# Performance work log

Measured on AMD Instinct MI355X. Metric: run time of the kernel, lower is better.

The kernel has to match this reference:

```python
import jax, jax.numpy as jnp
import numpy as np

NFRAMES, BS, LATENT = 196, 128, 1024
E = 16            # number of object types (experts)
NJOINTS = 128     # max joints -> padded width
NFEATS = 6
INPUT_FEATS = NJOINTS * NFEATS  # 768


def setup_inputs() -> dict:
    key = jax.random.key(0)
    k1, k2, k3, k4 = jax.random.split(key, 4)
    output = jax.random.normal(k1, (NFRAMES, BS, LATENT), dtype=jnp.float32)
    object_types = jax.random.randint(k2, (BS,), 0, E)
    # stacked per-type Linear params, zero-padded to INPUT_FEATS
    W = jax.random.normal(k3, (E, LATENT, INPUT_FEATS), dtype=jnp.float32) * (1.0 / np.sqrt(LATENT))
    b = jax.random.normal(k4, (E, INPUT_FEATS), dtype=jnp.float32) * 0.01
    # valid joints per type in [8, NJOINTS]
    joint_counts = jax.random.randint(jax.random.fold_in(key, 7), (E,), 8, NJOINTS + 1)
    return {"output": output, "object_types": object_types, "W": W, "b": b,
            "joint_counts": joint_counts}


def reference(output, object_types, W, b, joint_counts):
    # per-expert valid output width and column mask [E, INPUT_FEATS]
    feat_counts = joint_counts * NFEATS
    col_mask = (jnp.arange(INPUT_FEATS)[None, :] < feat_counts[:, None]).astype(output.dtype)
    # gather per-sample expert params: Wg [BS, LATENT, F], bg/mg [BS, F]
    Wg = W[object_types]
    bg = b[object_types]
    mg = col_mask[object_types]
    # y[t,b,f] = sum_d output[t,b,d] * Wg[b,d,f] + bg[b,f], zero-padded past valid width
    y = (jnp.einsum('tbd,bdf->tbf', output, Wg) + bg[None]) * mg[None]
    y = y.reshape(NFRAMES, BS, NJOINTS, NFEATS)
    return jnp.transpose(y, (1, 2, 3, 0))  # (bs, njoints, nfeats, nframes)
```

## Files before the change

kernel.cpp:

```cpp
#include <hip/hip_runtime.h>
#include <hip/hip_bf16.h>


#define NFRAMES 196
#define TPAD    208
#define BSZ     128
#define DLAT    1024
#define FIN     768
#define BM      128
#define BK      32
#define KSTEPS  (DLAT / BK)
#define MTILES  (FIN / BM)
#define NFRAG   (TPAD / 16)
#define NTHREADS 256

typedef short bf16x8 __attribute__((ext_vector_type(8)));
typedef short s16x4  __attribute__((ext_vector_type(4)));
typedef float f32x4  __attribute__((ext_vector_type(4)));

__device__ __forceinline__ int swz(int r) { return ((r >> 2) & 3) ^ ((r >> 1) & 1); }

__device__ __forceinline__ short f2bf(float f) {
    __hip_bfloat16 h = __float2bfloat16(f);
    return __builtin_bit_cast(short, h);
}

#define BAR() do { asm volatile("s_waitcnt lgkmcnt(0)" ::: "memory"); \
                   __builtin_amdgcn_s_barrier(); } while (0)

__global__ __launch_bounds__(NTHREADS, 2)
void fused_expert_gemm(const float* __restrict__ X,
                       const int*   __restrict__ otypes,
                       const float* __restrict__ W,
                       const float* __restrict__ Bias,
                       const int*   __restrict__ jc,
                       float*       __restrict__ out)
{
    __shared__ short As[BM * BK];
    __shared__ short Bs[TPAD * BK];

    const int hw      = blockIdx.x;
    const int logical = (hw & 7) * ((MTILES * BSZ) / 8) + (hw >> 3);
    const int b       = logical / MTILES;
    const int mt      = logical - b * MTILES;
    const int m0      = mt * BM;

    const int tid = threadIdx.x;
    const int e   = otypes[b];

    const int kb = tid >> 5;
    const int mb = tid & 31;
    const int kq = tid & 7;
    const int rp = tid >> 3;

    const f32x4* __restrict__ Xv = reinterpret_cast<const f32x4*>(X);
    const f32x4* __restrict__ Wv = reinterpret_cast<const f32x4*>(W);
    const f32x4 fzero = {0.f, 0.f, 0.f, 0.f};

    f32x4 wa[4];
    f32x4 xb[7];

    const int wave = tid >> 6;
    const int lane = tid & 63;
    const int lr   = lane & 15;
    const int g    = lane >> 4;

    f32x4 acc[2][NFRAG];
    #pragma unroll
    for (int i = 0; i < 2; ++i)
        #pragma unroll
        for (int j = 0; j < NFRAG; ++j) acc[i][j] = fzero;

    auto load_stage = [&](int k0) {
        #pragma unroll
        for (int i = 0; i < 4; ++i)
            wa[i] = Wv[(size_t)(e * DLAT + k0 + kb * 4 + i) * (FIN / 4) + (m0 >> 2) + mb];
        #pragma unroll
        for (int p = 0; p < 7; ++p) {
            const int n = p * 32 + rp;
            if (n < NFRAMES)
                xb[p] = Xv[((size_t)n * BSZ + b) * (DLAT / 4) + (k0 >> 2) + kq];
            else
                xb[p] = fzero;
        }
    };

    auto write_stage = [&]() {
        #pragma unroll
        for (int j = 0; j < 4; ++j) {
            const int mm = (mb + j) & 3;
            const int m  = mb * 4 + mm;
            s16x4 v;
            v[0] = f2bf(wa[0][mm]); v[1] = f2bf(wa[1][mm]);
            v[2] = f2bf(wa[2][mm]); v[3] = f2bf(wa[3][mm]);
            const int ea = m * 32 + (((kb >> 1) ^ swz(m)) << 3) + (kb & 1) * 4;
            *reinterpret_cast<s16x4*>(&As[ea]) = v;
        }
        #pragma unroll
        for (int p = 0; p < 7; ++p) {
            const int n = p * 32 + rp;
            if (n < TPAD) {
                s16x4 v;
                v[0] = f2bf(xb[p][0]); v[1] = f2bf(xb[p][1]);
                v[2] = f2bf(xb[p][2]); v[3] = f2bf(xb[p][3]);
                const int ea = n * 32 + (((kq >> 1) ^ swz(n)) << 3) + (kq & 1) * 4;
                *reinterpret_cast<s16x4*>(&Bs[ea]) = v;
            }
        }
    };

    load_stage(0);

    #pragma unroll 1
    for (int ks = 0; ks < KSTEPS; ++ks) {
        BAR();
        write_stage();
        if (ks + 1 < KSTEPS)
            load_stage((ks + 1) * BK);
        BAR();

        const int ma0 = wave * 32 + lr;
        const int ma1 = ma0 + 16;
        bf16x8 a0 = *reinterpret_cast<const bf16x8*>(&As[ma0 * 32 + ((g ^ swz(ma0)) << 3)]);
        bf16x8 a1 = *reinterpret_cast<const bf16x8*>(&As[ma1 * 32 + ((g ^ swz(ma1)) << 3)]);
        #pragma unroll
        for (int nf = 0; nf < NFRAG; ++nf) {
            const int nr = nf * 16 + lr;
            bf16x8 bf = *reinterpret_cast<const bf16x8*>(&Bs[nr * 32 + ((g ^ swz(nr)) << 3)]);
            acc[0][nf] = __builtin_amdgcn_mfma_f32_16x16x32_bf16(a0, bf, acc[0][nf], 0, 0, 0);
            acc[1][nf] = __builtin_amdgcn_mfma_f32_16x16x32_bf16(a1, bf, acc[1][nf], 0, 0, 0);
        }
    }

    const int   fcb   = jc[e] * 6;
    const float* biasE = Bias + e * FIN;
    float*       outB  = out + (size_t)b * (FIN * NFRAMES);

    #pragma unroll
    for (int mf = 0; mf < 2; ++mf) {
        #pragma unroll
        for (int r = 0; r < 4; ++r) {
            const int fcol = m0 + wave * 32 + mf * 16 + g * 4 + r;
            const float bv = biasE[fcol];
            const bool valid = fcol < fcb;
            #pragma unroll
            for (int nf = 0; nf < NFRAG; ++nf) {
                const int t = nf * 16 + lr;
                if (t < NFRAMES)
                    outB[fcol * NFRAMES + t] = valid ? (acc[mf][nf][r] + bv) : 0.f;
            }
        }
    }
}

extern "C" void kernel_launch(void* const* d_in, const int* in_sizes, int n_in,
                              void* d_out, int out_size, void* d_ws, size_t ws_size,
                              hipStream_t stream) {
    const float* X    = (const float*)d_in[0];
    const int*   ot   = (const int*)d_in[1];
    const float* W    = (const float*)d_in[2];
    const float* Bias = (const float*)d_in[3];
    const int*   jc   = (const int*)d_in[4];
    float*       out  = (float*)d_out;

    dim3 grid(MTILES * BSZ);
    dim3 block(NTHREADS);
    hipLaunchKernelGGL(fused_expert_gemm, grid, block, 0, stream,
                       X, ot, W, Bias, jc, out);
}
```

Measured before the change: 91.16 us.

## Retile expert GEMM to 96-column blocks with 2x2 wave grid

Changes the block tile from 128 output features by 208 frames to 96 by 224, with waves arranged 2x2 so each wave computes 48x112 (3x7 MFMA fragments) instead of 32x208. This gives 1024 blocks instead of 768 and a squarer per-wave tile, so each LDS fragment load feeds more MFMAs. The X staging switches to 8-wide loads and 16-byte LDS stores with a new swizzle, and LDS addresses are precomputed. The trade-offs are idle W-loading threads (only 24 of 32 columns active), extra padded frames computed, and more accumulator registers.

```diff
diff --git a/kernel.cpp b/kernel.cpp
--- a/kernel.cpp
+++ b/kernel.cpp
@@ -3,22 +3,22 @@
 
 
 #define NFRAMES 196
-#define TPAD    208
+#define TPAD    224
 #define BSZ     128
 #define DLAT    1024
 #define FIN     768
-#define BM      128
+#define BM      96
 #define BK      32
 #define KSTEPS  (DLAT / BK)
 #define MTILES  (FIN / BM)
-#define NFRAG   (TPAD / 16)
 #define NTHREADS 256
 
 typedef short bf16x8 __attribute__((ext_vector_type(8)));
+typedef short s16x8  __attribute__((ext_vector_type(8)));
 typedef short s16x4  __attribute__((ext_vector_type(4)));
 typedef float f32x4  __attribute__((ext_vector_type(4)));
 
-__device__ __forceinline__ int swz(int r) { return ((r >> 2) & 3) ^ ((r >> 1) & 1); }
+__device__ __forceinline__ int swz(int r) { return ((r >> 1) & 3) ^ ((r >> 3) & 3); }
 
 __device__ __forceinline__ short f2bf(float f) {
     __hip_bfloat16 h = __float2bfloat16(f);
@@ -41,70 +41,102 @@
 
     const int hw      = blockIdx.x;
     const int logical = (hw & 7) * ((MTILES * BSZ) / 8) + (hw >> 3);
-    const int b       = logical / MTILES;
-    const int mt      = logical - b * MTILES;
+    const int b       = logical >> 3;
+    const int mt      = logical & 7;
     const int m0      = mt * BM;
 
-    const int tid = threadIdx.x;
-    const int e   = otypes[b];
-
-    const int kb = tid >> 5;
-    const int mb = tid & 31;
-    const int kq = tid & 7;
-    const int rp = tid >> 3;
-
-    const f32x4* __restrict__ Xv = reinterpret_cast<const f32x4*>(X);
-    const f32x4* __restrict__ Wv = reinterpret_cast<const f32x4*>(W);
-    const f32x4 fzero = {0.f, 0.f, 0.f, 0.f};
-
-    f32x4 wa[4];
-    f32x4 xb[7];
-
+    const int tid  = threadIdx.x;
+    const int e    = otypes[b];
     const int wave = tid >> 6;
     const int lane = tid & 63;
     const int lr   = lane & 15;
-    const int g    = lane >> 4;
-
-    f32x4 acc[2][NFRAG];
-    #pragma unroll
-    for (int i = 0; i < 2; ++i)
-        #pragma unroll
-        for (int j = 0; j < NFRAG; ++j) acc[i][j] = fzero;
-
-    auto load_stage = [&](int k0) {
-        #pragma unroll
-        for (int i = 0; i < 4; ++i)
-            wa[i] = Wv[(size_t)(e * DLAT + k0 + kb * 4 + i) * (FIN / 4) + (m0 >> 2) + mb];
-        #pragma unroll
-        for (int p = 0; p < 7; ++p) {
-            const int n = p * 32 + rp;
-            if (n < NFRAMES)
-                xb[p] = Xv[((size_t)n * BSZ + b) * (DLAT / 4) + (k0 >> 2) + kq];
-            else
-                xb[p] = fzero;
+    const int g    = (lane >> 4) & 3;
+    const int wr   = wave >> 1;
+    const int wc   = wave & 1;
+
+    const int mb   = tid & 31;
+    const int kb   = tid >> 5;
+    const bool aact = (mb < 24);
+    const int ko = tid & 3;
+    const int rw = tid >> 2;
+
+    const f32x4* __restrict__ Xv = reinterpret_cast<const f32x4*>(X);
+    const f32x4* __restrict__ Wv = reinterpret_cast<const f32x4*>(W);
+    const f32x4 fz = {0.f, 0.f, 0.f, 0.f};
+
+    f32x4 wa[4];
+    f32x4 xb[4][2];
+
+    int idxA[3], idxB[7];
+    #pragma unroll
+    for (int f = 0; f < 3; ++f) {
+        const int ma = wr * 48 + f * 16 + lr;
+        idxA[f] = ma * BK + 8 * (g ^ swz(ma));
+    }
+    #pragma unroll
+    for (int nf = 0; nf < 7; ++nf) {
+        const int nr = wc * 112 + nf * 16 + lr;
+        idxB[nf] = nr * BK + 8 * (g ^ swz(nr));
+    }
+    int idxAw[4];
+    #pragma unroll
+    for (int j = 0; j < 4; ++j) {
+        const int r = (mb + j) & 3;
+        const int m = mb * 4 + r;
+        idxAw[j] = m * BK + 8 * (((kb >> 1) & 3) ^ swz(m)) + (kb & 1) * 4;
+    }
+    int idxBw[4];
+    #pragma unroll
+    for (int p = 0; p < 4; ++p) {
+        const int n = p * 64 + rw;
+        idxBw[p] = n * BK + 8 * (ko ^ swz(n));
+    }
+
+    f32x4 acc[3][7];
+    #pragma unroll
+    for (int f = 0; f < 3; ++f)
+        #pragma unroll
+        for (int nf = 0; nf < 7; ++nf) acc[f][nf] = fz;
+
+    auto load_stage = [&](int kk) {
+        if (aact) {
+            #pragma unroll
+            for (int i = 0; i < 4; ++i)
+                wa[i] = Wv[(e * DLAT + kk + kb * 4 + i) * (FIN / 4) + (m0 >> 2) + mb];
+        }
+        #pragma unroll
+        for (int p = 0; p < 4; ++p) {
+            const int n = p * 64 + rw;
+            if (n < NFRAMES) {
+                const int base = (n * BSZ + b) * (DLAT / 4) + (kk >> 2) + ko * 2;
+                xb[p][0] = Xv[base];
+                xb[p][1] = Xv[base + 1];
+            } else {
+                xb[p][0] = fz; xb[p][1] = fz;
+            }
         }
     };
 
     auto write_stage = [&]() {
-        #pragma unroll
-        for (int j = 0; j < 4; ++j) {
-            const int mm = (mb + j) & 3;
-            const int m  = mb * 4 + mm;
-            s16x4 v;
-            v[0] = f2bf(wa[0][mm]); v[1] = f2bf(wa[1][mm]);
-            v[2] = f2bf(wa[2][mm]); v[3] = f2bf(wa[3][mm]);
-            const int ea = m * 32 + (((kb >> 1) ^ swz(m)) << 3) + (kb & 1) * 4;
-            *reinterpret_cast<s16x4*>(&As[ea]) = v;
-        }
-        #pragma unroll
-        for (int p = 0; p < 7; ++p) {
-            const int n = p * 32 + rp;
-            if (n < TPAD) {
+        if (aact) {
+            #pragma unroll
+            for (int j = 0; j < 4; ++j) {
+                const int r = (mb + j) & 3;
                 s16x4 v;
-                v[0] = f2bf(xb[p][0]); v[1] = f2bf(xb[p][1]);
-                v[2] = f2bf(xb[p][2]); v[3] = f2bf(xb[p][3]);
-                const int ea = n * 32 + (((kq >> 1) ^ swz(n)) << 3) + (kq & 1) * 4;
-                *reinterpret_cast<s16x4*>(&Bs[ea]) = v;
+                v[0] = f2bf(wa[0][r]); v[1] = f2bf(wa[1][r]);
+                v[2] = f2bf(wa[2][r]); v[3] = f2bf(wa[3][r]);
+                *reinterpret_cast<s16x4*>(&As[idxAw[j]]) = v;
+            }
+        }
+        #pragma unroll
+        for (int p = 0; p < 4; ++p) {
+            if (p * 64 + rw < TPAD) {
+                s16x8 v;
+                v[0] = f2bf(xb[p][0][0]); v[1] = f2bf(xb[p][0][1]);
+                v[2] = f2bf(xb[p][0][2]); v[3] = f2bf(xb[p][0][3]);
+                v[4] = f2bf(xb[p][1][0]); v[5] = f2bf(xb[p][1][1]);
+                v[6] = f2bf(xb[p][1][2]); v[7] = f2bf(xb[p][1][3]);
+                *reinterpret_cast<s16x8*>(&Bs[idxBw[p]]) = v;
             }
         }
     };
@@ -119,35 +151,35 @@
             load_stage((ks + 1) * BK);
         BAR();
 
-        const int ma0 = wave * 32 + lr;
-        const int ma1 = ma0 + 16;
-        bf16x8 a0 = *reinterpret_cast<const bf16x8*>(&As[ma0 * 32 + ((g ^ swz(ma0)) << 3)]);
-        bf16x8 a1 = *reinterpret_cast<const bf16x8*>(&As[ma1 * 32 + ((g ^ swz(ma1)) << 3)]);
-        #pragma unroll
-        for (int nf = 0; nf < NFRAG; ++nf) {
-            const int nr = nf * 16 + lr;
-            bf16x8 bf = *reinterpret_cast<const bf16x8*>(&Bs[nr * 32 + ((g ^ swz(nr)) << 3)]);
-            acc[0][nf] = __builtin_amdgcn_mfma_f32_16x16x32_bf16(a0, bf, acc[0][nf], 0, 0, 0);
-            acc[1][nf] = __builtin_amdgcn_mfma_f32_16x16x32_bf16(a1, bf, acc[1][nf], 0, 0, 0);
-        }
-    }
-
-    const int   fcb   = jc[e] * 6;
+        bf16x8 af[3];
+        #pragma unroll
+        for (int f = 0; f < 3; ++f)
+            af[f] = *reinterpret_cast<const bf16x8*>(&As[idxA[f]]);
+        #pragma unroll
+        for (int nf = 0; nf < 7; ++nf) {
+            bf16x8 bv = *reinterpret_cast<const bf16x8*>(&Bs[idxB[nf]]);
+            #pragma unroll
+            for (int f = 0; f < 3; ++f)
+                acc[f][nf] = __builtin_amdgcn_mfma_f32_16x16x32_bf16(af[f], bv, acc[f][nf], 0, 0, 0);
+        }
+    }
+
+    const int    fcb   = jc[e] * 6;
     const float* biasE = Bias + e * FIN;
     float*       outB  = out + (size_t)b * (FIN * NFRAMES);
 
     #pragma unroll
-    for (int mf = 0; mf < 2; ++mf) {
-        #pragma unroll
-        for (int r = 0; r < 4; ++r) {
-            const int fcol = m0 + wave * 32 + mf * 16 + g * 4 + r;
-            const float bv = biasE[fcol];
-            const bool valid = fcol < fcb;
-            #pragma unroll
-            for (int nf = 0; nf < NFRAG; ++nf) {
-                const int t = nf * 16 + lr;
+    for (int f = 0; f < 3; ++f) {
+        #pragma unroll
+        for (int rr = 0; rr < 4; ++rr) {
+            const int fcol  = m0 + wr * 48 + f * 16 + g * 4 + rr;
+            const float bv  = biasE[fcol];
+            const bool  val = fcol < fcb;
+            #pragma unroll
+            for (int nf = 0; nf < 7; ++nf) {
+                const int t = wc * 112 + nf * 16 + lr;
                 if (t < NFRAMES)
-                    outB[fcol * NFRAMES + t] = valid ? (acc[mf][nf][r] + bv) : 0.f;
+                    outB[fcol * NFRAMES + t] = val ? (acc[f][nf][rr] + bv) : 0.f;
             }
         }
     }
```

Result: slower. 105.9 us (+16.2%).
